# Optimization experiments

Hardware: AMD Instinct MI355X
Metric: run time of the kernel (lower is better)

Reference implementation:

```python
import jax, jax.numpy as jnp
import numpy as np

NODES = 81
NODE_DIM = 2
IN_DIM = NODES * NODE_DIM  # 162
D = 256
H = 16
HD = D // H
DFF = 2048
T, B, E = 1024, 8, 648


def _layernorm(x, w, b, eps=1e-5):
    m = x.mean(-1, keepdims=True)
    v = x.var(-1, keepdims=True)
    return (x - m) / jnp.sqrt(v + eps) * w + b


def setup_inputs() -> dict:
    key = jax.random.key(0)
    ks = jax.random.split(key, 12)
    s = 0.02
    W = lambda k, shape: jax.random.normal(k, shape, jnp.float32) * s
    return {
        "src": jax.random.normal(ks[0], (T, B, IN_DIM), jnp.float32),
        "edge_index": jax.random.randint(ks[1], (2, E), 0, NODES),
        "gcn_w": W(ks[2], (NODE_DIM, NODE_DIM)),
        "gcn_b": jnp.zeros((NODE_DIM,), jnp.float32),
        "fc_w": W(ks[3], (IN_DIM, D)),
        "fc_b": jnp.zeros((D,), jnp.float32),
        "wq": W(ks[4], (D, D)), "bq": jnp.zeros((D,), jnp.float32),
        "wk": W(ks[5], (D, D)), "bk": jnp.zeros((D,), jnp.float32),
        "wv": W(ks[6], (D, D)), "bv": jnp.zeros((D,), jnp.float32),
        "wo": W(ks[7], (D, D)), "bo": jnp.zeros((D,), jnp.float32),
        "ln1_w": jnp.ones((D,), jnp.float32), "ln1_b": jnp.zeros((D,), jnp.float32),
        "ffn_w1": W(ks[8], (D, DFF)), "ffn_b1": jnp.zeros((DFF,), jnp.float32),
        "ffn_w2": W(ks[9], (DFF, D)), "ffn_b2": jnp.zeros((D,), jnp.float32),
        "ln2_w": jnp.ones((D,), jnp.float32), "ln2_b": jnp.zeros((D,), jnp.float32),
        "dec_w": W(ks[10], (D, IN_DIM)), "dec_b": jnp.zeros((IN_DIM,), jnp.float32),
    }


def reference(src, edge_index, gcn_w, gcn_b, fc_w, fc_b, wq, bq, wk, bk, wv, bv,
              wo, bo, ln1_w, ln1_b, ffn_w1, ffn_b1, ffn_w2, ffn_b2, ln2_w, ln2_b,
              dec_w, dec_b):
    t, b, _ = src.shape
    # ---- batched GCNConv(2,2): all T*B tiny graphs share one adjacency ----
    # src[t,b] = [in_flow(81), out_flow(81)] -> node features [81, 2]
    xg = jnp.swapaxes(src.reshape(t, b, NODE_DIM, NODES), -1, -2)  # [T,B,81,2]
    row, col = edge_index[0], edge_index[1]
    A = jnp.zeros((NODES, NODES), src.dtype).at[col, row].add(1.0)
    A = A + jnp.eye(NODES, dtype=src.dtype)          # add self-loops
    deg = A.sum(1)
    dinv = jnp.where(deg > 0, 1.0 / jnp.sqrt(deg), 0.0)
    A_hat = dinv[:, None] * A * dinv[None, :]        # D^-1/2 (A+I) D^-1/2
    hg = jnp.einsum('ij,tbjc->tbic', A_hat, xg @ gcn_w) + gcn_b  # [T,B,81,2]
    # gcn_output.transpose(0,1).view(-1): channel-major flatten
    src2 = jnp.swapaxes(hg, -1, -2).reshape(t, b, IN_DIM)
    # ---- fc + positional encoding ----
    x = src2 @ fc_w + fc_b  # [T,B,D]
    pos = jnp.arange(t, dtype=jnp.float32)[:, None]
    div = jnp.exp(jnp.arange(0, D, 2, dtype=jnp.float32) * (-np.log(10000.0) / D))
    pe = jnp.zeros((t, D), x.dtype).at[:, 0::2].set(jnp.sin(pos * div))
    pe = pe.at[:, 1::2].set(jnp.cos(pos * div))
    x = x + pe[:, None, :]
    # ---- TransformerEncoderLayer (post-norm, relu, causal mask, eval) ----
    q = (x @ wq + bq).reshape(t, b, H, HD)
    k = (x @ wk + bk).reshape(t, b, H, HD)
    v = (x @ wv + bv).reshape(t, b, H, HD)
    scores = jnp.einsum('tbhd,sbhd->bhts', q, k) / jnp.sqrt(jnp.asarray(HD, x.dtype))
    causal = jnp.tril(jnp.ones((t, t), bool))
    scores = jnp.where(causal, scores, jnp.finfo(x.dtype).min)
    attn = jax.nn.softmax(scores, axis=-1)
    ctx = jnp.einsum('bhts,sbhd->tbhd', attn, v).reshape(t, b, D) @ wo + bo
    x = _layernorm(x + ctx, ln1_w, ln1_b)
    ff = jax.nn.relu(x @ ffn_w1 + ffn_b1) @ ffn_w2 + ffn_b2
    x = _layernorm(x + ff, ln2_w, ln2_b)
    return x @ dec_w + dec_b  # [T,B,162]
```

## Files before the change

kernel.cpp:

```cpp
#include <hip/hip_runtime.h>
#include <math.h>

#define T_    1024
#define B_    8
#define D_    256
#define H_    16
#define HD_   16
#define DFF_  2048
#define NODES_ 81
#define INDIM_ 162
#define E_    648
#define M_    (T_*B_)

typedef __bf16 bf16x8 __attribute__((ext_vector_type(8)));
typedef float  f32x4  __attribute__((ext_vector_type(4)));
typedef unsigned short ushort_t;
typedef unsigned int   uint_t;

union bfpack { bf16x8 v; uint_t u[4]; };

__device__ __forceinline__ ushort_t f2bf(float f) {
    union { float f; uint_t u; } c; c.f = f;
    uint_t u = c.u;
    uint_t r = u + 0x7fffu + ((u >> 16) & 1u);
    return (ushort_t)(r >> 16);
}

__device__ __forceinline__ uint_t fbits(float f) {
    union { float f; uint_t u; } c; c.f = f;
    return c.u;
}

__device__ __forceinline__ bf16x8 zero8() {
    bf16x8 v;
#pragma unroll
    for (int e = 0; e < 8; e++) v[e] = (__bf16)0.0f;
    return v;
}

__device__ __forceinline__ void gload_lds16(const void* g, void* l) {
    __builtin_amdgcn_global_load_lds(
        (const __attribute__((address_space(1))) void*)g,
        (__attribute__((address_space(3))) void*)l, 16, 0, 0);
}

__device__ __forceinline__ void trans_tile(
        const float* __restrict__ in, ushort_t* __restrict__ out,
        float (*tile)[33], int K, int N, int Kp, int bx, int by) {
    int k0 = bx * 32, n0 = by * 32;
    int tx = threadIdx.x & 31, ty = threadIdx.x >> 5;
#pragma unroll
    for (int i = 0; i < 4; i++) {
        int r = k0 + ty + i * 8, c = n0 + tx;
        tile[ty + i * 8][tx] = (r < K && c < N) ? in[(size_t)r * N + c] : 0.f;
    }
    __syncthreads();
#pragma unroll
    for (int i = 0; i < 4; i++) {
        int r = n0 + ty + i * 8, c = k0 + tx;
        out[(size_t)r * Kp + c] = f2bf(tile[tx][ty + i * 8]);
    }
}

__global__ __launch_bounds__(256) void prep_all(
        const int* __restrict__ edge, const float* __restrict__ gcn_w,
        const float* __restrict__ gcn_b, const float* __restrict__ fc_w,
        const float* __restrict__ fc_b, const float* __restrict__ src,
        const float* __restrict__ wq, const float* __restrict__ wk,
        const float* __restrict__ wv, const float* __restrict__ wo,
        const float* __restrict__ dec_w, const float* __restrict__ w1,
        const float* __restrict__ w2,
        const float* __restrict__ bq, const float* __restrict__ bk,
        const float* __restrict__ bv,
        ushort_t* __restrict__ weffT, float* __restrict__ beff,
        ushort_t* __restrict__ srcb,
        ushort_t* __restrict__ wqkvT, ushort_t* __restrict__ woT,
        ushort_t* __restrict__ dwT, ushort_t* __restrict__ w1T,
        ushort_t* __restrict__ w2T, float* __restrict__ qkvbias) {
    __shared__ float A[NODES_ * NODES_];
    __shared__ float dinv[NODES_];
    __shared__ float tile[32][33];
    int bid = blockIdx.x;
    int tid = threadIdx.x;
    if (bid < 82) {
        for (int i = tid; i < NODES_ * NODES_; i += 256) A[i] = 0.f;
        __syncthreads();
        for (int e = tid; e < E_; e += 256) {
            int r = edge[e];
            int c = edge[E_ + e];
            atomicAdd(&A[c * NODES_ + r], 1.0f);
        }
        __syncthreads();
        if (tid < NODES_) A[tid * NODES_ + tid] += 1.0f;
        __syncthreads();
        if (tid < NODES_) {
            float s = 0.f;
            for (int k = 0; k < NODES_; k++) s += A[tid * NODES_ + k];
            dinv[tid] = (s > 0.f) ? rsqrtf(s) : 0.f;
        }
        __syncthreads();
        int d = tid, j = bid;
        if (j < NODES_) {
            float s0 = 0.f, s1 = 0.f;
            for (int i = 0; i < NODES_; i++) {
                float a = dinv[i] * A[i * NODES_ + j] * dinv[j];
                s0 += a * fc_w[(0 * NODES_ + i) * D_ + d];
                s1 += a * fc_w[(1 * NODES_ + i) * D_ + d];
            }
            weffT[d * 192 + j]          = f2bf(gcn_w[0] * s0 + gcn_w[1] * s1);
            weffT[d * 192 + NODES_ + j] = f2bf(gcn_w[2] * s0 + gcn_w[3] * s1);
        } else {
            float t0 = 0.f, t1 = 0.f;
            for (int i = 0; i < NODES_; i++) {
                t0 += fc_w[(0 * NODES_ + i) * D_ + d];
                t1 += fc_w[(1 * NODES_ + i) * D_ + d];
            }
            beff[d] = fc_b[d] + gcn_b[0] * t0 + gcn_b[1] * t1;
            for (int c = INDIM_; c < 192; c++) weffT[d * 192 + c] = 0;
        }
    } else if (bid < 1426) {
        int l = bid - 82;
        if (l < 64)        trans_tile(wq,    wqkvT,          tile, D_,   D_,     D_,   l & 7,  l >> 3);
        else if (l < 128)  trans_tile(wk,    wqkvT + 65536,  tile, D_,   D_,     D_,   (l-64) & 7,  (l-64) >> 3);
        else if (l < 192)  trans_tile(wv,    wqkvT + 131072, tile, D_,   D_,     D_,   (l-128) & 7, (l-128) >> 3);
        else if (l < 256)  trans_tile(wo,    woT,            tile, D_,   D_,     D_,   (l-192) & 7, (l-192) >> 3);
        else if (l < 320)  trans_tile(dec_w, dwT,            tile, D_,   INDIM_, D_,   (l-256) & 7, (l-256) >> 3);
        else if (l < 832)  trans_tile(w1,    w1T,            tile, D_,   DFF_,   D_,   (l-320) & 7, (l-320) >> 3);
        else               trans_tile(w2,    w2T,            tile, DFF_, D_,     DFF_, (l-832) & 63, (l-832) >> 6);
    } else if (bid == 1426) {
#pragma unroll
        for (int k = 0; k < 3; k++) {
            int i = k * 256 + tid;
            qkvbias[i] = (i < 256) ? bq[i] : ((i < 512) ? bk[i - 256] : bv[i - 512]);
        }
    } else {
        int r = bid - 1427;
        if (tid < 192)
            srcb[(size_t)r * 192 + tid] =
                (tid < INDIM_) ? f2bf(src[(size_t)r * INDIM_ + tid]) : (ushort_t)0;
    }
}

enum { EP_PE = 0, EP_QKV = 1, EP_PLAIN = 2, EP_RELU = 3, EP_DEC = 4, EP_PART = 5 };

template <int EPI, int TM, int KS>
__global__ __launch_bounds__(256) void gemm_bf16(
        const ushort_t* __restrict__ A, const ushort_t* __restrict__ BT,
        const float* __restrict__ bias, float* __restrict__ Cf,
        ushort_t* __restrict__ Cb, int M, int N, int K) {
    __shared__ ushort_t sA[TM * 64];
    __shared__ ushort_t sB[128 * 64];
    int tid = threadIdx.x;
    int w = tid >> 6, lane = tid & 63;
    int cc = lane & 15, q = lane >> 4;
    int bm = blockIdx.y * TM, bn = blockIdx.x * 128;
    int part = (KS > 1) ? blockIdx.z : 0;
    int kbeg = part * (K / KS), kend = kbeg + K / KS;

    int srow = (lane >> 3);
    int sslot = lane & 7;

    const int NJ = (TM == 128) ? 4 : 2;
    int mbase = (TM == 128) ? ((w >> 1) * 64) : 0;
    int nbase = (TM == 128) ? ((w & 1) * 64) : (w * 32);

    f32x4 acc[4][NJ];
#pragma unroll
    for (int i = 0; i < 4; i++)
#pragma unroll
        for (int j = 0; j < NJ; j++)
#pragma unroll
            for (int e = 0; e < 4; e++) acc[i][j][e] = 0.f;

    for (int k0 = kbeg; k0 < kend; k0 += 64) {
        if (TM == 128) {
#pragma unroll
            for (int i = 0; i < 4; i++) {
                int r = w * 32 + i * 8 + srow;
                const ushort_t* ga = A + (size_t)(bm + r) * K + k0 + ((sslot ^ (r & 7)) * 8);
                gload_lds16(ga, &sA[(w * 32 + i * 8) * 64]);
            }
        } else {
#pragma unroll
            for (int i = 0; i < 2; i++) {
                int r = w * 16 + i * 8 + srow;
                const ushort_t* ga = A + (size_t)(bm + r) * K + k0 + ((sslot ^ (r & 7)) * 8);
                gload_lds16(ga, &sA[(w * 16 + i * 8) * 64]);
            }
        }
#pragma unroll
        for (int i = 0; i < 4; i++) {
            int r = w * 32 + i * 8 + srow;
            const ushort_t* gb = BT + (size_t)(bn + r) * K + k0 + ((sslot ^ (r & 7)) * 8);
            gload_lds16(gb, &sB[(w * 32 + i * 8) * 64]);
        }
        __syncthreads();
#pragma unroll
        for (int ks = 0; ks < 2; ks++) {
            bf16x8 af[4], bfr[NJ];
#pragma unroll
            for (int i = 0; i < 4; i++) {
                int m = mbase + i * 16 + cc;
                int off = m * 64 + (((ks * 4 + q) ^ (cc & 7)) * 8);
                af[i] = *(const bf16x8*)&sA[off];
            }
#pragma unroll
            for (int j = 0; j < NJ; j++) {
                int n = nbase + j * 16 + cc;
                int off = n * 64 + (((ks * 4 + q) ^ (cc & 7)) * 8);
                bfr[j] = *(const bf16x8*)&sB[off];
            }
#pragma unroll
            for (int i = 0; i < 4; i++)
#pragma unroll
                for (int j = 0; j < NJ; j++)
                    acc[i][j] = __builtin_amdgcn_mfma_f32_16x16x32_bf16(af[i], bfr[j], acc[i][j], 0, 0, 0);
        }
        __syncthreads();
    }

#pragma unroll
    for (int i = 0; i < 4; i++) {
#pragma unroll
        for (int j = 0; j < NJ; j++) {
            int col = bn + nbase + j * 16 + cc;
            float bv = 0.f;
            if (EPI == EP_DEC) bv = (col < INDIM_) ? bias[col] : 0.f;
            else if (EPI != EP_PART) bv = bias[col];
#pragma unroll
            for (int reg = 0; reg < 4; reg++) {
                int row = bm + mbase + i * 16 + q * 4 + reg;
                float v = acc[i][j][reg] + bv;
                if (EPI == EP_PE) {
                    int t = row >> 3;
                    float freq = __expf((float)(col & ~1) * (-9.210340371976184f / 256.f));
                    float ang = (float)t * freq;
                    v += (col & 1) ? __cosf(ang) : __sinf(ang);
                    Cf[(size_t)row * N + col] = v;
                    Cb[(size_t)row * N + col] = f2bf(v);
                } else if (EPI == EP_QKV) {
                    int t = row >> 3, b = row & 7;
                    int nn = col & 255, which = col >> 8;
                    int h = nn >> 4, hd = nn & 15;
                    Cb[(size_t)which * 2097152 +
                       ((size_t)((b * H_ + h) * T_ + t)) * HD_ + hd] = f2bf(v);
                } else if (EPI == EP_PLAIN) {
                    Cf[(size_t)row * N + col] = v;
                } else if (EPI == EP_RELU) {
                    v = fmaxf(v, 0.f);
                    Cb[(size_t)row * N + col] = f2bf(v);
                } else if (EPI == EP_DEC) {
                    if (col < INDIM_) Cf[(size_t)row * INDIM_ + col] = v;
                } else if (EPI == EP_PART) {
                    Cf[(size_t)part * M * N + (size_t)row * N + col] = v;
                }
            }
        }
    }
}

__global__ __launch_bounds__(256) void attn_mfma(
        const ushort_t* __restrict__ Qb, const ushort_t* __restrict__ Kb,
        const ushort_t* __restrict__ Vb, ushort_t* __restrict__ ctxb) {
    int qc = 7 - blockIdx.x;
    int bh = blockIdx.y;
    int tid = threadIdx.x;
    int w = tid >> 6, lane = tid & 63;
    int cc = lane & 15, q = lane >> 4;
    int qb0 = qc * 128;

    __shared__ ushort_t VTs[2][16 * 72];

    const ushort_t* Qp = Qb + (size_t)bh * (T_ * HD_);
    const ushort_t* Kp = Kb + (size_t)bh * (T_ * HD_);
    const ushort_t* Vp = Vb + (size_t)bh * (T_ * HD_);

    bf16x8 qf[2];
#pragma unroll
    for (int i = 0; i < 2; i++) {
        if (q < 2)
            qf[i] = *(const bf16x8*)&Qp[(size_t)(qb0 + w * 32 + i * 16 + cc) * HD_ + q * 8];
        else
            qf[i] = zero8();
    }

    bf16x8 ones8;
#pragma unroll
    for (int e = 0; e < 8; e++) ones8[e] = (__bf16)1.0f;

    f32x4 ot[2], ls[2];
#pragma unroll
    for (int i = 0; i < 2; i++)
#pragma unroll
        for (int e = 0; e < 4; e++) { ot[i][e] = 0.f; ls[i][e] = 0.f; }

    int ntiles = 2 * (qc + 1);
    int qmaxw = qb0 + w * 32 + 31;

    for (int kb = 0; kb < ntiles; kb++) {
        ushort_t* vbuf = VTs[kb & 1];
        if (tid < 128) {
            int r = tid >> 1, half = tid & 1;
            bf16x8 vv = *(const bf16x8*)&Vp[(size_t)(kb * 64 + r) * HD_ + half * 8];
#pragma unroll
            for (int e = 0; e < 8; e++)
                vbuf[(half * 8 + e) * 72 + r] = ((const ushort_t*)&vv)[e];
        }
        __syncthreads();
        if (kb * 64 > qmaxw) continue;

        f32x4 s[2][4];
#pragma unroll
        for (int j = 0; j < 4; j++) {
            bf16x8 kf;
            if (q < 2)
                kf = *(const bf16x8*)&Kp[(size_t)(kb * 64 + j * 16 + cc) * HD_ + q * 8];
            else
                kf = zero8();
#pragma unroll
            for (int i = 0; i < 2; i++) {
                f32x4 z;
#pragma unroll
                for (int e = 0; e < 4; e++) z[e] = 0.f;
                s[i][j] = __builtin_amdgcn_mfma_f32_16x16x32_bf16(kf, qf[i], z, 0, 0, 0);
            }
        }

#pragma unroll
        for (int j = 0; j < 4; j++) {
            bfpack af;
            const uint_t* vt = (const uint_t*)&vbuf[cc * 72 + j * 16 + q * 4];
            af.u[0] = vt[0]; af.u[1] = vt[1]; af.u[2] = 0u; af.u[3] = 0u;
            int key0 = kb * 64 + j * 16 + q * 4;
#pragma unroll
            for (int i = 0; i < 2; i++) {
                int qrow = qb0 + w * 32 + i * 16 + cc;
                float p0 = __expf(s[i][j][0] * 0.25f);
                float p1 = __expf(s[i][j][1] * 0.25f);
                float p2 = __expf(s[i][j][2] * 0.25f);
                float p3 = __expf(s[i][j][3] * 0.25f);
                if (key0 + 0 > qrow) p0 = 0.f;
                if (key0 + 1 > qrow) p1 = 0.f;
                if (key0 + 2 > qrow) p2 = 0.f;
                if (key0 + 3 > qrow) p3 = 0.f;
                bfpack pf;
                pf.u[0] = (fbits(p0) >> 16) | (fbits(p1) & 0xffff0000u);
                pf.u[1] = (fbits(p2) >> 16) | (fbits(p3) & 0xffff0000u);
                pf.u[2] = 0u; pf.u[3] = 0u;
                ot[i] = __builtin_amdgcn_mfma_f32_16x16x32_bf16(af.v, pf.v, ot[i], 0, 0, 0);
                ls[i] = __builtin_amdgcn_mfma_f32_16x16x32_bf16(ones8, pf.v, ls[i], 0, 0, 0);
            }
        }
    }

    int b = bh >> 4, h = bh & 15;
#pragma unroll
    for (int i = 0; i < 2; i++) {
        int t = qb0 + w * 32 + i * 16 + cc;
        float linv = 1.f / ls[i][0];
        ushort4 ov;
        ov.x = f2bf(ot[i][0] * linv);
        ov.y = f2bf(ot[i][1] * linv);
        ov.z = f2bf(ot[i][2] * linv);
        ov.w = f2bf(ot[i][3] * linv);
        *(ushort4*)&ctxb[((size_t)t * B_ + b) * D_ + h * HD_ + q * 4] = ov;
    }
}

template <int NP, bool HASB>
__global__ __launch_bounds__(256) void ln_kernel(
        const float* __restrict__ X, const float* __restrict__ P0,
        const float* __restrict__ P1, const float* __restrict__ RB,
        const float* __restrict__ w, const float* __restrict__ b,
        float* __restrict__ out, ushort_t* __restrict__ outb) {
    int wv = threadIdx.x >> 6, lane = threadIdx.x & 63;
    int row = blockIdx.x * 4 + wv;
    int c = lane * 4;
    const float4 x4 = *(const float4*)&X[(size_t)row * D_ + c];
    const float4 p4 = *(const float4*)&P0[(size_t)row * D_ + c];
    float v0 = x4.x + p4.x, v1 = x4.y + p4.y, v2 = x4.z + p4.z, v3 = x4.w + p4.w;
    if (NP == 2) {
        const float4 q4 = *(const float4*)&P1[(size_t)row * D_ + c];
        v0 += q4.x; v1 += q4.y; v2 += q4.z; v3 += q4.w;
    }
    if (HASB) {
        const float4 r4 = *(const float4*)&RB[c];
        v0 += r4.x; v1 += r4.y; v2 += r4.z; v3 += r4.w;
    }
    float s  = v0 + v1 + v2 + v3;
    float sq = v0 * v0 + v1 * v1 + v2 * v2 + v3 * v3;
    for (int off = 32; off; off >>= 1) {
        s  += __shfl_xor(s, off);
        sq += __shfl_xor(sq, off);
    }
    float mean = s * (1.f / 256.f);
    float var  = sq * (1.f / 256.f) - mean * mean;
    float rstd = rsqrtf(var + 1e-5f);
    float o0 = (v0 - mean) * rstd * w[c + 0] + b[c + 0];
    float o1 = (v1 - mean) * rstd * w[c + 1] + b[c + 1];
    float o2 = (v2 - mean) * rstd * w[c + 2] + b[c + 2];
    float o3 = (v3 - mean) * rstd * w[c + 3] + b[c + 3];
    float4 o; o.x = o0; o.y = o1; o.z = o2; o.w = o3;
    *(float4*)&out[(size_t)row * D_ + c] = o;
    ushort4 ob;
    ob.x = f2bf(o0); ob.y = f2bf(o1); ob.z = f2bf(o2); ob.w = f2bf(o3);
    *(ushort4*)&outb[(size_t)row * D_ + c] = ob;
}

extern "C" void kernel_launch(void* const* d_in, const int* in_sizes, int n_in,
                              void* d_out, int out_size, void* d_ws, size_t ws_size,
                              hipStream_t stream) {
    (void)in_sizes; (void)n_in; (void)out_size; (void)ws_size;
    const float* src     = (const float*)d_in[0];
    const int*   edge    = (const int*)d_in[1];
    const float* gcn_w   = (const float*)d_in[2];
    const float* gcn_b   = (const float*)d_in[3];
    const float* fc_w    = (const float*)d_in[4];
    const float* fc_b    = (const float*)d_in[5];
    const float* wq      = (const float*)d_in[6];
    const float* bq      = (const float*)d_in[7];
    const float* wk      = (const float*)d_in[8];
    const float* bk      = (const float*)d_in[9];
    const float* wv      = (const float*)d_in[10];
    const float* bv      = (const float*)d_in[11];
    const float* wo      = (const float*)d_in[12];
    const float* bo      = (const float*)d_in[13];
    const float* ln1_w   = (const float*)d_in[14];
    const float* ln1_b   = (const float*)d_in[15];
    const float* ffn_w1  = (const float*)d_in[16];
    const float* ffn_b1  = (const float*)d_in[17];
    const float* ffn_w2  = (const float*)d_in[18];
    const float* ffn_b2  = (const float*)d_in[19];
    const float* ln2_w   = (const float*)d_in[20];
    const float* ln2_b   = (const float*)d_in[21];
    const float* dec_w   = (const float*)d_in[22];
    const float* dec_b   = (const float*)d_in[23];
    float* out = (float*)d_out;

    float* ws = (float*)d_ws;
    float* beff    = ws;
    float* qkvbias = ws + 256;
    float* x0      = ws + 1024;
    float* tmp     = x0  + 2097152;
    float* tmp2    = tmp + 2097152;
    float* x1      = tmp2 + 2097152;
    float* x2s     = x1  + 2097152;
    ushort_t* ub   = (ushort_t*)(ws + 10486784);
    ushort_t* srcb = ub;
    ushort_t* x0b  = ub + 1572864;
    ushort_t* x1b  = x0b + 2097152;
    ushort_t* x2b  = x1b + 2097152;
    ushort_t* ctxb = x2b + 2097152;
    ushort_t* hb   = ctxb + 2097152;
    ushort_t* qkvb = hb + 16777216;
    ushort_t* weffT= qkvb + 6291456;
    ushort_t* wqkvT= weffT + 49152;
    ushort_t* woT  = wqkvT + 196608;
    ushort_t* w1T  = woT + 65536;
    ushort_t* w2T  = w1T + 524288;
    ushort_t* dwT  = w2T + 524288;

    prep_all<<<9619, 256, 0, stream>>>(edge, gcn_w, gcn_b, fc_w, fc_b, src,
                                       wq, wk, wv, wo, dec_w, ffn_w1, ffn_w2,
                                       bq, bk, bv, weffT, beff, srcb,
                                       wqkvT, woT, dwT, w1T, w2T, qkvbias);

    gemm_bf16<EP_PE, 64, 1><<<dim3(2, 128), 256, 0, stream>>>(srcb, weffT, beff, x0, x0b, M_, D_, 192);
    gemm_bf16<EP_QKV, 64, 1><<<dim3(6, 128), 256, 0, stream>>>(x0b, wqkvT, qkvbias, nullptr, qkvb, M_, 768, D_);
    attn_mfma<<<dim3(8, 128), 256, 0, stream>>>(qkvb, qkvb + 2097152, qkvb + 4194304, ctxb);
    gemm_bf16<EP_PLAIN, 64, 1><<<dim3(2, 128), 256, 0, stream>>>(ctxb, woT, bo, tmp, nullptr, M_, D_, D_);
    ln_kernel<1, false><<<2048, 256, 0, stream>>>(x0, tmp, nullptr, nullptr, ln1_w, ln1_b, x1, x1b);
    gemm_bf16<EP_RELU, 128, 1><<<dim3(16, 64), 256, 0, stream>>>(x1b, w1T, ffn_b1, nullptr, hb, M_, DFF_, D_);
    gemm_bf16<EP_PART, 64, 2><<<dim3(2, 128, 2), 256, 0, stream>>>(hb, w2T, nullptr, tmp, nullptr, M_, D_, DFF_);
    ln_kernel<2, true><<<2048, 256, 0, stream>>>(x1, tmp, tmp2, ffn_b2, ln2_w, ln2_b, x2s, x2b);
    gemm_bf16<EP_DEC, 64, 1><<<dim3(2, 128), 256, 0, stream>>>(x2b, dwT, dec_b, out, nullptr, M_, D_, D_);
}
```

Before: 256.2 us.

## Split causal attention over key chunks with a separate reduction kernel

Attention blocks are split into 20 slots per head, each covering up to four 64-key tiles of a 128-query chunk, so the load no longer depends on the triangular shape of causal attention. Partial unnormalised outputs and row sums are written to fp32 scratch, reusing the FFN hidden buffer, and a new reduction kernel sums them and normalises into bf16 context. The row-sum MFMA with a ones vector is replaced by scalar adds of truncated probabilities plus a shuffle reduction. The cost is an extra launch and extra global traffic for the partials.

```diff
diff --git a/kernel.cpp b/kernel.cpp
--- a/kernel.cpp
+++ b/kernel.cpp
@@ -29,6 +29,11 @@
 __device__ __forceinline__ uint_t fbits(float f) {
     union { float f; uint_t u; } c; c.f = f;
     return c.u;
+}
+
+__device__ __forceinline__ float truncbf(float f) {
+    union { uint_t u; float f; } c; c.u = fbits(f) & 0xffff0000u;
+    return c.f;
 }
 
 __device__ __forceinline__ bf16x8 zero8() {
@@ -261,13 +266,20 @@
 
 __global__ __launch_bounds__(256) void attn_mfma(
         const ushort_t* __restrict__ Qb, const ushort_t* __restrict__ Kb,
-        const ushort_t* __restrict__ Vb, ushort_t* __restrict__ ctxb) {
-    int qc = 7 - blockIdx.x;
+        const ushort_t* __restrict__ Vb, float* __restrict__ partO,
+        float* __restrict__ partL) {
+    const int qc_of[20] = {0,1,2,2,3,3,4,4,4,5,5,5,6,6,6,6,7,7,7,7};
+    const int kp_of[20] = {0,0,0,1,0,1,0,1,2,0,1,2,0,1,2,3,0,1,2,3};
+    int slot = blockIdx.x;
+    int qc = qc_of[slot], kp = kp_of[slot];
     int bh = blockIdx.y;
     int tid = threadIdx.x;
     int w = tid >> 6, lane = tid & 63;
     int cc = lane & 15, q = lane >> 4;
     int qb0 = qc * 128;
+    int kbeg = kp * 4;
+    int kend = 2 * (qc + 1);
+    if (kend > kbeg + 4) kend = kbeg + 4;
 
     __shared__ ushort_t VTs[2][16 * 72];
 
@@ -284,20 +296,16 @@
             qf[i] = zero8();
     }
 
-    bf16x8 ones8;
-#pragma unroll
-    for (int e = 0; e < 8; e++) ones8[e] = (__bf16)1.0f;
-
-    f32x4 ot[2], ls[2];
+    f32x4 ot[2];
+    float lacc[2] = {0.f, 0.f};
 #pragma unroll
     for (int i = 0; i < 2; i++)
 #pragma unroll
-        for (int e = 0; e < 4; e++) { ot[i][e] = 0.f; ls[i][e] = 0.f; }
-
-    int ntiles = 2 * (qc + 1);
+        for (int e = 0; e < 4; e++) ot[i][e] = 0.f;
+
     int qmaxw = qb0 + w * 32 + 31;
 
-    for (int kb = 0; kb < ntiles; kb++) {
+    for (int kb = kbeg; kb < kend; kb++) {
         ushort_t* vbuf = VTs[kb & 1];
         if (tid < 128) {
             int r = tid >> 1, half = tid & 1;
@@ -348,23 +356,52 @@
                 pf.u[1] = (fbits(p2) >> 16) | (fbits(p3) & 0xffff0000u);
                 pf.u[2] = 0u; pf.u[3] = 0u;
                 ot[i] = __builtin_amdgcn_mfma_f32_16x16x32_bf16(af.v, pf.v, ot[i], 0, 0, 0);
-                ls[i] = __builtin_amdgcn_mfma_f32_16x16x32_bf16(ones8, pf.v, ls[i], 0, 0, 0);
-            }
-        }
-    }
-
-    int b = bh >> 4, h = bh & 15;
+                lacc[i] += truncbf(p0) + truncbf(p1) + truncbf(p2) + truncbf(p3);
+            }
+        }
+    }
+
+    int base = (bh * 20 + slot) * 128;
 #pragma unroll
     for (int i = 0; i < 2; i++) {
-        int t = qb0 + w * 32 + i * 16 + cc;
-        float linv = 1.f / ls[i][0];
-        ushort4 ov;
-        ov.x = f2bf(ot[i][0] * linv);
-        ov.y = f2bf(ot[i][1] * linv);
-        ov.z = f2bf(ot[i][2] * linv);
-        ov.w = f2bf(ot[i][3] * linv);
-        *(ushort4*)&ctxb[((size_t)t * B_ + b) * D_ + h * HD_ + q * 4] = ov;
-    }
+        float l0 = lacc[i];
+        l0 += __shfl_xor(l0, 16);
+        l0 += __shfl_xor(l0, 32);
+        int row = w * 32 + i * 16 + cc;
+        *(f32x4*)&partO[((size_t)(base + row)) * 16 + q * 4] = ot[i];
+        if (q == 0) partL[base + row] = l0;
+    }
+}
+
+__global__ __launch_bounds__(256) void attn_reduce(
+        const float* __restrict__ partO, const float* __restrict__ partL,
+        ushort_t* __restrict__ ctxb) {
+    const int cum[9] = {0, 1, 2, 4, 6, 9, 12, 16, 20};
+    int qc = blockIdx.x, bh = blockIdx.y;
+    int row = threadIdx.x >> 1, dh = threadIdx.x & 1;
+    int p0 = cum[qc], p1 = cum[qc + 1];
+    float o[8];
+#pragma unroll
+    for (int e = 0; e < 8; e++) o[e] = 0.f;
+    float l = 0.f;
+    for (int p = p0; p < p1; p++) {
+        size_t base = ((size_t)bh * 20 + p) * 128 + row;
+        const float4 a = *(const float4*)&partO[base * 16 + dh * 8];
+        const float4 b4 = *(const float4*)&partO[base * 16 + dh * 8 + 4];
+        o[0] += a.x; o[1] += a.y; o[2] += a.z; o[3] += a.w;
+        o[4] += b4.x; o[5] += b4.y; o[6] += b4.z; o[7] += b4.w;
+        l += partL[base];
+    }
+    float inv = 1.f / l;
+    int t = qc * 128 + row, b = bh >> 4, h = bh & 15;
+    ushort_t* op = ctxb + ((size_t)t * B_ + b) * D_ + h * HD_ + dh * 8;
+    ushort4 u0, u1;
+    u0.x = f2bf(o[0] * inv); u0.y = f2bf(o[1] * inv);
+    u0.z = f2bf(o[2] * inv); u0.w = f2bf(o[3] * inv);
+    u1.x = f2bf(o[4] * inv); u1.y = f2bf(o[5] * inv);
+    u1.z = f2bf(o[6] * inv); u1.w = f2bf(o[7] * inv);
+    *(ushort4*)&op[0] = u0;
+    *(ushort4*)&op[4] = u1;
 }
 
 template <int NP, bool HASB>
@@ -459,6 +496,8 @@
     ushort_t* w1T  = woT + 65536;
     ushort_t* w2T  = w1T + 524288;
     ushort_t* dwT  = w2T + 524288;
+    float* partO = (float*)hb;
+    float* partL = partO + 5242880;
 
     prep_all<<<9619, 256, 0, stream>>>(edge, gcn_w, gcn_b, fc_w, fc_b, src,
                                        wq, wk, wv, wo, dec_w, ffn_w1, ffn_w2,
@@ -467,7 +506,8 @@
 
     gemm_bf16<EP_PE, 64, 1><<<dim3(2, 128), 256, 0, stream>>>(srcb, weffT, beff, x0, x0b, M_, D_, 192);
     gemm_bf16<EP_QKV, 64, 1><<<dim3(6, 128), 256, 0, stream>>>(x0b, wqkvT, qkvbias, nullptr, qkvb, M_, 768, D_);
-    attn_mfma<<<dim3(8, 128), 256, 0, stream>>>(qkvb, qkvb + 2097152, qkvb + 4194304, ctxb);
+    attn_mfma<<<dim3(20, 128), 256, 0, stream>>>(qkvb, qkvb + 2097152, qkvb + 4194304, partO, partL);
+    attn_reduce<<<dim3(8, 128), 256, 0, stream>>>(partO, partL, ctxb);
     gemm_bf16<EP_PLAIN, 64, 1><<<dim3(2, 128), 256, 0, stream>>>(ctxb, woT, bo, tmp, nullptr, M_, D_, D_);
     ln_kernel<1, false><<<2048, 256, 0, stream>>>(x0, tmp, nullptr, nullptr, ln1_w, ln1_b, x1, x1b);
     gemm_bf16<EP_RELU, 128, 1><<<dim3(16, 64), 256, 0, stream>>>(x1b, w1T, ffn_b1, nullptr, hb, M_, DFF_, D_);
```

Result: faster. 240.8 us (-6.0%).
